# Kernel optimization log

Hardware: AMD Instinct MI355X
Metric: run time of the kernel (lower is better)

## Reference

```python
import jax, jax.numpy as jnp
import numpy as np

D_MODEL = 1024
NUM_HEADS = 16
HEAD_DIM = D_MODEL // NUM_HEADS
B, S, L_CACHE = 2, 1024, 1024


def setup_inputs() -> dict:
    key = jax.random.key(0)
    ks = jax.random.split(key, 12)
    sc = 1.0 / np.sqrt(D_MODEL)
    return {
        "x": jax.random.normal(ks[0], (B, S, D_MODEL), jnp.float32),
        "cache_k": jax.random.normal(ks[1], (B, NUM_HEADS, L_CACHE, HEAD_DIM), jnp.float32),
        "cache_v": jax.random.normal(ks[2], (B, NUM_HEADS, L_CACHE, HEAD_DIM), jnp.float32),
        "Wq": jax.random.normal(ks[3], (D_MODEL, D_MODEL), jnp.float32) * sc,
        "bq": jax.random.normal(ks[4], (D_MODEL,), jnp.float32) * 0.01,
        "Wk": jax.random.normal(ks[5], (D_MODEL, D_MODEL), jnp.float32) * sc,
        "bk": jax.random.normal(ks[6], (D_MODEL,), jnp.float32) * 0.01,
        "Wv": jax.random.normal(ks[7], (D_MODEL, D_MODEL), jnp.float32) * sc,
        "bv": jax.random.normal(ks[8], (D_MODEL,), jnp.float32) * 0.01,
        "Wo": jax.random.normal(ks[9], (D_MODEL, D_MODEL), jnp.float32) * sc,
        "bo": jax.random.normal(ks[10], (D_MODEL,), jnp.float32) * 0.01,
    }


def reference(x, cache_k, cache_v, Wq, bq, Wk, bk, Wv, bv, Wo, bo):
    b, s, d = x.shape
    h, hd = NUM_HEADS, HEAD_DIM
    # torch Linear: y = x @ W^T + b
    def proj(W, bias):
        y = jnp.einsum('bsd,ed->bse', x, W) + bias
        return y.reshape(b, s, h, hd).transpose(0, 2, 1, 3)  # [B,H,S,hd]
    Q = proj(Wq, bq)
    K = jnp.concatenate([cache_k, proj(Wk, bk)], axis=2)  # [B,H,T,hd]
    V = jnp.concatenate([cache_v, proj(Wv, bv)], axis=2)
    T = K.shape[2]
    scores = jnp.einsum('bhqd,bhkd->bhqk', Q, K) / jnp.sqrt(jnp.float32(hd))
    # causal mask with cache offset: query i sees keys j <= i + (T - s)
    offset = T - s
    q_idx = jnp.arange(s)[:, None]
    k_idx = jnp.arange(T)[None, :]
    mask = k_idx > (q_idx + offset)  # [S,T], True = masked
    scores = jnp.where(mask[None, None], -jnp.inf, scores)
    attn = jax.nn.softmax(scores, axis=-1)
    out = jnp.einsum('bhqk,bhkd->bhqd', attn, V)
    out = out.transpose(0, 2, 1, 3).reshape(b, s, d)
    return jnp.einsum('bsd,ed->bse', out, Wo) + bo
```

## Files before the change

### kernel.cpp

```cpp
#include <hip/hip_runtime.h>
#include <hip/hip_bf16.h>
#include <stdint.h>

typedef __bf16 bf16;
typedef __bf16 bf16x4 __attribute__((ext_vector_type(4)));
typedef __bf16 bf16x8 __attribute__((ext_vector_type(8)));
typedef float  f32x4  __attribute__((ext_vector_type(4)));

#define DEV __device__ __forceinline__

#define BB 2
#define HH 16
#define SS 1024
#define DD 1024
#define HD 64
#define LC 1024
#define TT 2048
#define OFFS 1024

DEV f32x4 mfma16(bf16x8 a, bf16x8 b, f32x4 c) {
    return __builtin_amdgcn_mfma_f32_16x16x32_bf16(a, b, c, 0, 0, 0);
}

DEV void async_load16(const bf16* g, bf16* lds) {
    auto gp = reinterpret_cast<const __attribute__((address_space(1))) void*>(
        reinterpret_cast<uintptr_t>(g));
    auto lp = reinterpret_cast<__attribute__((address_space(3))) void*>(
        reinterpret_cast<uintptr_t>(lds));
    __builtin_amdgcn_global_load_lds(gp, lp, 16, 0, 0);
}

__global__ __launch_bounds__(256) void cvt_all(
    const float* __restrict__ x,  bf16* __restrict__ xb,
    const float* __restrict__ w0, const float* __restrict__ w1,
    const float* __restrict__ w2, const float* __restrict__ w3,
    bf16* __restrict__ d0, bf16* __restrict__ d1,
    bf16* __restrict__ d2, bf16* __restrict__ d3,
    const float* __restrict__ ck, bf16* __restrict__ Kf,
    const float* __restrict__ cv, bf16* __restrict__ Vt) {
    __shared__ float tile[64][65];
    const int bid = blockIdx.x;
    const int tid = threadIdx.x;
    if (bid < 8192) {
        const float* s;
        bf16* d;
        int i;
        if (bid < 2048) {
            s = x; d = xb; i = bid * 256 + tid;
        } else if (bid < 6144) {
            int which = (bid - 2048) >> 10;
            s = which == 0 ? w0 : which == 1 ? w1 : which == 2 ? w2 : w3;
            d = which == 0 ? d0 : which == 1 ? d1 : which == 2 ? d2 : d3;
            i = ((bid - 2048) & 1023) * 256 + tid;
        } else {
            int ii = (bid - 6144) * 256 + tid;
            int bh  = ii >> 14;
            int rem = ii & 16383;
            float4 v = ((const float4*)ck)[ii];
            bf16x4 o;
            o[0] = (bf16)v.x; o[1] = (bf16)v.y; o[2] = (bf16)v.z; o[3] = (bf16)v.w;
            ((bf16x4*)(Kf + (size_t)bh * TT * HD))[rem] = o;
            return;
        }
        float4 v = ((const float4*)s)[i];
        bf16x4 o;
        o[0] = (bf16)v.x; o[1] = (bf16)v.y; o[2] = (bf16)v.z; o[3] = (bf16)v.w;
        ((bf16x4*)d)[i] = o;
    } else {
        int rem = bid - 8192;
        int bh = rem >> 4;
        int t0 = (rem & 15) * 64;
        int c4 = (tid & 15) * 4;
        int rr = tid >> 4;
        const float* src = cv + ((size_t)bh * LC + t0) * HD;
#pragma unroll
        for (int p = 0; p < 4; ++p) {
            int t = rr + p * 16;
            float4 v = *(const float4*)(src + (size_t)t * HD + c4);
            tile[c4 + 0][t] = v.x; tile[c4 + 1][t] = v.y;
            tile[c4 + 2][t] = v.z; tile[c4 + 3][t] = v.w;
        }
        __syncthreads();
        bf16* dst = Vt + (size_t)bh * HD * TT + t0;
#pragma unroll
        for (int p = 0; p < 4; ++p) {
            int d = rr + p * 16;
            int tc = (tid & 15) * 4;
            bf16x4 o;
            o[0] = (bf16)tile[d][tc + 0]; o[1] = (bf16)tile[d][tc + 1];
            o[2] = (bf16)tile[d][tc + 2]; o[3] = (bf16)tile[d][tc + 3];
            *(bf16x4*)(dst + (size_t)d * TT + tc) = o;
        }
    }
}

__global__ __launch_bounds__(256) void gemm_nt(
    const bf16* __restrict__ A, const bf16* __restrict__ W,
    const float* __restrict__ bq, const float* __restrict__ bk,
    const float* __restrict__ bv, const float* __restrict__ bo,
    bf16* __restrict__ Qb, bf16* __restrict__ Kf, bf16* __restrict__ Vt,
    float* __restrict__ Out, int is_oproj) {
    const int tid  = threadIdx.x;
    const int wv   = tid >> 6;
    const int lane = tid & 63;
    const int l16  = lane & 15;
    const int quad = lane >> 4;
    const int m0 = blockIdx.y * 64;
    const int n0 = blockIdx.x * 128;
    const int mode = is_oproj ? 3 : (n0 >> 10);
    const float* bias = (mode == 0) ? bq : (mode == 1) ? bk : (mode == 2) ? bv : bo;

    __shared__ __align__(16) bf16 As[2][64 * 64];
    __shared__ __align__(16) bf16 Bs[2][128 * 64];

    f32x4 acc[4][2];
#pragma unroll
    for (int i = 0; i < 4; ++i)
#pragma unroll
        for (int j = 0; j < 2; ++j) {
            f32x4 z = {0.f, 0.f, 0.f, 0.f};
            acc[i][j] = z;
        }

    auto stage = [&](int k0, int b) {
#pragma unroll
        for (int k = 0; k < 2; ++k) {
            int seg = k * 256 + tid;
            int row = seg >> 3;
            int c   = (seg & 7) ^ (row & 7);
            async_load16(A + (size_t)(m0 + row) * 1024 + k0 + c * 8, &As[b][seg * 8]);
        }
#pragma unroll
        for (int k = 0; k < 4; ++k) {
            int seg = k * 256 + tid;
            int row = seg >> 3;
            int c   = (seg & 7) ^ (row & 7);
            async_load16(W + (size_t)(n0 + row) * 1024 + k0 + c * 8, &Bs[b][seg * 8]);
        }
    };

    stage(0, 0);

    for (int it = 0; it < 16; ++it) {
        __syncthreads();
        const bf16* Ab = &As[it & 1][0];
        const bf16* Bb = &Bs[it & 1][0];
        if (it + 1 < 16) stage((it + 1) * 64, (it + 1) & 1);

#pragma unroll
        for (int kk = 0; kk < 2; ++kk) {
            bf16x8 af[4], bfr[2];
#pragma unroll
            for (int i = 0; i < 4; ++i) {
                int row = i * 16 + l16;
                int slot = (kk * 4 + quad) ^ (row & 7);
                af[i] = *(const bf16x8*)(Ab + (row * 8 + slot) * 8);
            }
#pragma unroll
            for (int j = 0; j < 2; ++j) {
                int row = wv * 32 + j * 16 + l16;
                int slot = (kk * 4 + quad) ^ (row & 7);
                bfr[j] = *(const bf16x8*)(Bb + (row * 8 + slot) * 8);
            }
#pragma unroll
            for (int i = 0; i < 4; ++i)
#pragma unroll
                for (int j = 0; j < 2; ++j)
                    acc[i][j] = mfma16(af[i], bfr[j], acc[i][j]);
        }
    }

#pragma unroll
    for (int i = 0; i < 4; ++i) {
#pragma unroll
        for (int j = 0; j < 2; ++j) {
            int n = n0 + wv * 32 + j * 16 + l16;
            float bval = bias[n & 1023];
#pragma unroll
            for (int r = 0; r < 4; ++r) {
                int m = m0 + i * 16 + quad * 4 + r;
                float v = acc[i][j][r] + bval;
                if (mode == 3) {
                    Out[(size_t)m * 1024 + n] = v;
                } else {
                    int b = m >> 10, s = m & 1023;
                    int h = (n & 1023) >> 6, d = n & 63;
                    int bh = b * HH + h;
                    if (mode == 0)
                        Qb[((size_t)bh * SS + s) * HD + d] = (bf16)v;
                    else if (mode == 1)
                        Kf[((size_t)bh * TT + LC + s) * HD + d] = (bf16)v;
                    else
                        Vt[((size_t)bh * HD + d) * TT + LC + s] = (bf16)v;
                }
            }
        }
    }
}

__global__ __launch_bounds__(256) void attn(const bf16* __restrict__ Qb,
                                            const bf16* __restrict__ Kf,
                                            const bf16* __restrict__ Vt,
                                            bf16* __restrict__ Ob) {
    const int i = blockIdx.x;
    const int bh = i & 31;
    const int qblk = (i < 256) ? (15 - (i >> 5)) : ((i >> 5) - 8);
    const int tid  = threadIdx.x;
    const int wv   = tid >> 6;
    const int qh   = wv & 1;
    const int kh   = wv >> 1;
    const int lane = tid & 63;
    const int l16  = lane & 15;
    const int quad = lane >> 4;
    const int qb   = qblk * 64;
    const int qw   = qb + qh * 32;
    const int kbase = kh * 64;

    const bf16* Qp = Qb + ((size_t)bh * SS + qw) * HD;
    const bf16* Kp = Kf + (size_t)bh * TT * HD;
    const bf16* Vp = Vt + (size_t)bh * HD * TT;

    __shared__ __align__(16) bf16 Ks[2][128 * 64];
    __shared__ __align__(16) bf16 Vs[2][64 * 128];

    bf16x8 qf[2][2];
#pragma unroll
    for (int qs = 0; qs < 2; ++qs)
#pragma unroll
        for (int dc = 0; dc < 2; ++dc)
            qf[qs][dc] = *(const bf16x8*)(Qp + (qs * 16 + l16) * HD + dc * 32 + quad * 8);

    float lsum[2] = {0.f, 0.f};
    f32x4 o[4][2];
#pragma unroll
    for (int dt = 0; dt < 4; ++dt)
#pragma unroll
        for (int qs = 0; qs < 2; ++qs) {
            f32x4 z = {0.f, 0.f, 0.f, 0.f};
            o[dt][qs] = z;
        }

    const int niters = qblk / 2 + 9;

    auto stage = [&](int tile, int b) {
        const int t0 = tile * 128;
#pragma unroll
        for (int j = 0; j < 4; ++j) {
            int seg = j * 256 + tid;
            int krow = seg >> 3;
            int kc   = (seg & 7) ^ (krow & 7);
            async_load16(Kp + (size_t)(t0 + krow) * HD + kc * 8, &Ks[b][seg * 8]);
            int drow = seg >> 4;
            int tc   = (seg & 15) ^ (drow & 15);
            async_load16(Vp + (size_t)drow * TT + t0 + tc * 8, &Vs[b][seg * 8]);
        }
    };

    stage(0, 0);

    const float C1 = 0.18033688f;
    const float C2 = -11.5415603f;

    for (int it = 0; it < niters; ++it) {
        __syncthreads();
        const bf16* Kb = &Ks[it & 1][0];
        const bf16* Vb = &Vs[it & 1][0];
        if (it + 1 < niters) stage(it + 1, (it + 1) & 1);

        const int t0 = it * 128;
        if (t0 + kbase > qw + 31 + OFFS) continue;
        const bool full = (t0 + kbase + 63 <= qw + OFFS);

        f32x4 s[4][2];
#pragma unroll
        for (int kt = 0; kt < 4; ++kt) {
            int row = kbase + kt * 16 + l16;
            int swz = row & 7;
            bf16x8 ka = *(const bf16x8*)(Kb + (row * 8 + (quad ^ swz)) * 8);
            bf16x8 kb = *(const bf16x8*)(Kb + (row * 8 + ((4 + quad) ^ swz)) * 8);
#pragma unroll
            for (int qs = 0; qs < 2; ++qs) {
                f32x4 z = {0.f, 0.f, 0.f, 0.f};
                z = mfma16(ka, qf[qs][0], z);
                z = mfma16(kb, qf[qs][1], z);
                s[kt][qs] = z;
            }
        }

        f32x4 p[4][2];
        if (full) {
#pragma unroll
            for (int kt = 0; kt < 4; ++kt)
#pragma unroll
                for (int qs = 0; qs < 2; ++qs)
#pragma unroll
                    for (int r = 0; r < 4; ++r)
                        p[kt][qs][r] = __builtin_amdgcn_exp2f(fmaf(s[kt][qs][r], C1, C2));
        } else {
#pragma unroll
            for (int qs = 0; qs < 2; ++qs) {
                const int qlim = qw + qs * 16 + l16 + OFFS - t0;
#pragma unroll
                for (int kt = 0; kt < 4; ++kt)
#pragma unroll
                    for (int r = 0; r < 4; ++r) {
                        int tl = kbase + kt * 16 + quad * 4 + r;
                        float e = __builtin_amdgcn_exp2f(fmaf(s[kt][qs][r], C1, C2));
                        p[kt][qs][r] = (tl <= qlim) ? e : 0.f;
                    }
            }
        }
#pragma unroll
        for (int qs = 0; qs < 2; ++qs)
#pragma unroll
            for (int kt = 0; kt < 4; ++kt)
                lsum[qs] += (p[kt][qs][0] + p[kt][qs][1]) + (p[kt][qs][2] + p[kt][qs][3]);

        bf16x8 pf[2][2];
#pragma unroll
        for (int kf = 0; kf < 2; ++kf)
#pragma unroll
            for (int qs = 0; qs < 2; ++qs)
#pragma unroll
                for (int j = 0; j < 4; ++j) {
                    pf[kf][qs][j]     = (bf16)p[kf * 2][qs][j];
                    pf[kf][qs][4 + j] = (bf16)p[kf * 2 + 1][qs][j];
                }

        const int q1 = quad >> 1;
        const int h4 = (quad & 1) * 4;
#pragma unroll
        for (int dt = 0; dt < 4; ++dt) {
            int row = dt * 16 + l16;
            int swz = row & 15;
#pragma unroll
            for (int kf = 0; kf < 2; ++kf) {
                int c0 = kh * 8 + kf * 4 + q1;
                bf16x4 v0 = *(const bf16x4*)(Vb + (row * 16 + (c0 ^ swz)) * 8 + h4);
                bf16x4 v1 = *(const bf16x4*)(Vb + (row * 16 + ((c0 + 2) ^ swz)) * 8 + h4);
                bf16x8 vf;
#pragma unroll
                for (int j = 0; j < 4; ++j) {
                    vf[j] = v0[j]; vf[4 + j] = v1[j];
                }
#pragma unroll
                for (int qs = 0; qs < 2; ++qs)
                    o[dt][qs] = mfma16(vf, pf[kf][qs], o[dt][qs]);
            }
        }
    }

#pragma unroll
    for (int qs = 0; qs < 2; ++qs) {
        lsum[qs] += __shfl_xor(lsum[qs], 16, 64);
        lsum[qs] += __shfl_xor(lsum[qs], 32, 64);
    }

    __syncthreads();
    float* So = (float*)&Ks[0][0];
    float* Sl = (float*)&Vs[0][0];
    if (kh == 1) {
#pragma unroll
        for (int dt = 0; dt < 4; ++dt)
#pragma unroll
            for (int qs = 0; qs < 2; ++qs)
#pragma unroll
                for (int r = 0; r < 4; ++r)
                    So[(dt * 8 + qs * 4 + r) * 128 + qh * 64 + lane] = o[dt][qs][r];
#pragma unroll
        for (int qs = 0; qs < 2; ++qs)
            Sl[qs * 128 + qh * 64 + lane] = lsum[qs];
    }
    __syncthreads();
    if (kh == 1) return;

#pragma unroll
    for (int dt = 0; dt < 4; ++dt)
#pragma unroll
        for (int qs = 0; qs < 2; ++qs)
#pragma unroll
            for (int r = 0; r < 4; ++r)
                o[dt][qs][r] += So[(dt * 8 + qs * 4 + r) * 128 + qh * 64 + lane];
    float rl[2];
#pragma unroll
    for (int qs = 0; qs < 2; ++qs)
        rl[qs] = 1.f / (lsum[qs] + Sl[qs * 128 + qh * 64 + lane]);

    const int b = bh >> 4, h = bh & 15;
#pragma unroll
    for (int qs = 0; qs < 2; ++qs) {
        const int q = qw + qs * 16 + l16;
        bf16* op = Ob + (((size_t)(b * SS + q) * HH) + h) * HD;
#pragma unroll
        for (int dt = 0; dt < 4; ++dt) {
            bf16x4 w;
#pragma unroll
            for (int r = 0; r < 4; ++r) w[r] = (bf16)(o[dt][qs][r] * rl[qs]);
            *(bf16x4*)(op + dt * 16 + quad * 4) = w;
        }
    }
}

extern "C" void kernel_launch(void* const* d_in, const int* in_sizes, int n_in,
                              void* d_out, int out_size, void* d_ws, size_t ws_size,
                              hipStream_t stream) {
    const float* x   = (const float*)d_in[0];
    const float* ck  = (const float*)d_in[1];
    const float* cv  = (const float*)d_in[2];
    const float* Wq  = (const float*)d_in[3];
    const float* bq  = (const float*)d_in[4];
    const float* Wk  = (const float*)d_in[5];
    const float* bk  = (const float*)d_in[6];
    const float* Wv  = (const float*)d_in[7];
    const float* bv  = (const float*)d_in[8];
    const float* Wo  = (const float*)d_in[9];
    const float* bo  = (const float*)d_in[10];
    float* out = (float*)d_out;

    char* ws = (char*)d_ws;
    bf16* xb  = (bf16*)(ws);
    bf16* wqb = (bf16*)(ws + ( 4u << 20));
    bf16* wkb = (bf16*)(ws + ( 6u << 20));
    bf16* wvb = (bf16*)(ws + ( 8u << 20));
    bf16* wob = (bf16*)(ws + (10u << 20));
    bf16* Qb  = (bf16*)(ws + (12u << 20));
    bf16* Kf  = (bf16*)(ws + (16u << 20));
    bf16* Vt  = (bf16*)(ws + (24u << 20));
    bf16* Ob  = (bf16*)(ws + (32u << 20));

    cvt_all<<<8704, 256, 0, stream>>>(x, xb, Wq, Wk, Wv, Wo, wqb, wkb, wvb, wob,
                                      ck, Kf, cv, Vt);

    gemm_nt<<<dim3(24, 32), 256, 0, stream>>>(xb, wqb, bq, bk, bv, bo,
                                              Qb, Kf, Vt, out, 0);
    attn<<<512, 256, 0, stream>>>(Qb, Kf, Vt, Ob);
    gemm_nt<<<dim3(8, 32), 256, 0, stream>>>(Ob, wob, bq, bk, bv, bo,
                                             Qb, Kf, Vt, out, 1);
}
```

Before: 159.5 us.

## Widen conversion vectors, add smaller-tile o-proj GEMM, simplify attention block order

The fp32-to-bf16 conversion kernel now handles eight elements per thread with 16-byte stores, which halves the number of blocks. The output projection moves to a dedicated kernel with 32-row tiles, so it launches twice as many blocks (512 instead of 256) to fill the GPU better. The projection-GEMM epilogue drops the o-proj branch. The attention block-to-query mapping changes from a zig-zag order to a plain descending order. That last change could alter load balance across the causal workload.

```diff
diff --git a/kernel.cpp b/kernel.cpp
--- a/kernel.cpp
+++ b/kernel.cpp
@@ -28,6 +28,13 @@
     auto lp = reinterpret_cast<__attribute__((address_space(3))) void*>(
         reinterpret_cast<uintptr_t>(lds));
     __builtin_amdgcn_global_load_lds(gp, lp, 16, 0, 0);
+}
+
+DEV bf16x8 cvt8(float4 a, float4 b) {
+    bf16x8 o;
+    o[0] = (bf16)a.x; o[1] = (bf16)a.y; o[2] = (bf16)a.z; o[3] = (bf16)a.w;
+    o[4] = (bf16)b.x; o[5] = (bf16)b.y; o[6] = (bf16)b.z; o[7] = (bf16)b.w;
+    return o;
 }
 
 __global__ __launch_bounds__(256) void cvt_all(
@@ -41,33 +48,31 @@
     __shared__ float tile[64][65];
     const int bid = blockIdx.x;
     const int tid = threadIdx.x;
-    if (bid < 8192) {
+    if (bid < 4096) {
         const float* s;
         bf16* d;
         int i;
-        if (bid < 2048) {
-            s = x; d = xb; i = bid * 256 + tid;
-        } else if (bid < 6144) {
-            int which = (bid - 2048) >> 10;
+        if (bid < 1024) {
+            s = x; d = xb; i = bid * 512 + tid * 2;
+        } else if (bid < 3072) {
+            int which = (bid - 1024) >> 9;
             s = which == 0 ? w0 : which == 1 ? w1 : which == 2 ? w2 : w3;
             d = which == 0 ? d0 : which == 1 ? d1 : which == 2 ? d2 : d3;
-            i = ((bid - 2048) & 1023) * 256 + tid;
+            i = ((bid - 1024) & 511) * 512 + tid * 2;
         } else {
-            int ii = (bid - 6144) * 256 + tid;
+            int ii = (bid - 3072) * 512 + tid * 2;
             int bh  = ii >> 14;
             int rem = ii & 16383;
-            float4 v = ((const float4*)ck)[ii];
-            bf16x4 o;
-            o[0] = (bf16)v.x; o[1] = (bf16)v.y; o[2] = (bf16)v.z; o[3] = (bf16)v.w;
-            ((bf16x4*)(Kf + (size_t)bh * TT * HD))[rem] = o;
+            float4 a = ((const float4*)ck)[ii];
+            float4 b = ((const float4*)ck)[ii + 1];
+            ((bf16x8*)(Kf + (size_t)bh * TT * HD))[rem >> 1] = cvt8(a, b);
             return;
         }
-        float4 v = ((const float4*)s)[i];
-        bf16x4 o;
-        o[0] = (bf16)v.x; o[1] = (bf16)v.y; o[2] = (bf16)v.z; o[3] = (bf16)v.w;
-        ((bf16x4*)d)[i] = o;
+        float4 a = ((const float4*)s)[i];
+        float4 b = ((const float4*)s)[i + 1];
+        ((bf16x8*)d)[i >> 1] = cvt8(a, b);
     } else {
-        int rem = bid - 8192;
+        int rem = bid - 4096;
         int bh = rem >> 4;
         int t0 = (rem & 15) * 64;
         int c4 = (tid & 15) * 4;
@@ -97,9 +102,8 @@
 __global__ __launch_bounds__(256) void gemm_nt(
     const bf16* __restrict__ A, const bf16* __restrict__ W,
     const float* __restrict__ bq, const float* __restrict__ bk,
-    const float* __restrict__ bv, const float* __restrict__ bo,
-    bf16* __restrict__ Qb, bf16* __restrict__ Kf, bf16* __restrict__ Vt,
-    float* __restrict__ Out, int is_oproj) {
+    const float* __restrict__ bv,
+    bf16* __restrict__ Qb, bf16* __restrict__ Kf, bf16* __restrict__ Vt) {
     const int tid  = threadIdx.x;
     const int wv   = tid >> 6;
     const int lane = tid & 63;
@@ -107,8 +111,8 @@
     const int quad = lane >> 4;
     const int m0 = blockIdx.y * 64;
     const int n0 = blockIdx.x * 128;
-    const int mode = is_oproj ? 3 : (n0 >> 10);
-    const float* bias = (mode == 0) ? bq : (mode == 1) ? bk : (mode == 2) ? bv : bo;
+    const int mode = n0 >> 10;
+    const float* bias = (mode == 0) ? bq : (mode == 1) ? bk : bv;
 
     __shared__ __align__(16) bf16 As[2][64 * 64];
     __shared__ __align__(16) bf16 Bs[2][128 * 64];
@@ -180,19 +184,100 @@
             for (int r = 0; r < 4; ++r) {
                 int m = m0 + i * 16 + quad * 4 + r;
                 float v = acc[i][j][r] + bval;
-                if (mode == 3) {
-                    Out[(size_t)m * 1024 + n] = v;
-                } else {
-                    int b = m >> 10, s = m & 1023;
-                    int h = (n & 1023) >> 6, d = n & 63;
-                    int bh = b * HH + h;
-                    if (mode == 0)
-                        Qb[((size_t)bh * SS + s) * HD + d] = (bf16)v;
-                    else if (mode == 1)
-                        Kf[((size_t)bh * TT + LC + s) * HD + d] = (bf16)v;
-                    else
-                        Vt[((size_t)bh * HD + d) * TT + LC + s] = (bf16)v;
-                }
+                int b = m >> 10, s = m & 1023;
+                int h = (n & 1023) >> 6, d = n & 63;
+                int bh = b * HH + h;
+                if (mode == 0)
+                    Qb[((size_t)bh * SS + s) * HD + d] = (bf16)v;
+                else if (mode == 1)
+                    Kf[((size_t)bh * TT + LC + s) * HD + d] = (bf16)v;
+                else
+                    Vt[((size_t)bh * HD + d) * TT + LC + s] = (bf16)v;
+            }
+        }
+    }
+}
+
+__global__ __launch_bounds__(256) void gemm_oproj(
+    const bf16* __restrict__ A, const bf16* __restrict__ W,
+    const float* __restrict__ bo, float* __restrict__ Out) {
+    const int tid  = threadIdx.x;
+    const int wv   = tid >> 6;
+    const int lane = tid & 63;
+    const int l16  = lane & 15;
+    const int quad = lane >> 4;
+    const int m0 = blockIdx.y * 32;
+    const int n0 = blockIdx.x * 128;
+
+    __shared__ __align__(16) bf16 As[2][32 * 64];
+    __shared__ __align__(16) bf16 Bs[2][128 * 64];
+
+    f32x4 acc[2][2];
+#pragma unroll
+    for (int i = 0; i < 2; ++i)
+#pragma unroll
+        for (int j = 0; j < 2; ++j) {
+            f32x4 z = {0.f, 0.f, 0.f, 0.f};
+            acc[i][j] = z;
+        }
+
+    auto stage = [&](int k0, int b) {
+        {
+            int seg = tid;
+            int row = seg >> 3;
+            int c   = (seg & 7) ^ (row & 7);
+            async_load16(A + (size_t)(m0 + row) * 1024 + k0 + c * 8, &As[b][seg * 8]);
+        }
+#pragma unroll
+        for (int k = 0; k < 4; ++k) {
+            int seg = k * 256 + tid;
+            int row = seg >> 3;
+            int c   = (seg & 7) ^ (row & 7);
+            async_load16(W + (size_t)(n0 + row) * 1024 + k0 + c * 8, &Bs[b][seg * 8]);
+        }
+    };
+
+    stage(0, 0);
+
+    for (int it = 0; it < 16; ++it) {
+        __syncthreads();
+        const bf16* Ab = &As[it & 1][0];
+        const bf16* Bb = &Bs[it & 1][0];
+        if (it + 1 < 16) stage((it + 1) * 64, (it + 1) & 1);
+
+#pragma unroll
+        for (int kk = 0; kk < 2; ++kk) {
+            bf16x8 af[2], bfr[2];
+#pragma unroll
+            for (int i = 0; i < 2; ++i) {
+                int row = i * 16 + l16;
+                int slot = (kk * 4 + quad) ^ (row & 7);
+                af[i] = *(const bf16x8*)(Ab + (row * 8 + slot) * 8);
+            }
+#pragma unroll
+            for (int j = 0; j < 2; ++j) {
+                int row = wv * 32 + j * 16 + l16;
+                int slot = (kk * 4 + quad) ^ (row & 7);
+                bfr[j] = *(const bf16x8*)(Bb + (row * 8 + slot) * 8);
+            }
+#pragma unroll
+            for (int i = 0; i < 2; ++i)
+#pragma unroll
+                for (int j = 0; j < 2; ++j)
+                    acc[i][j] = mfma16(af[i], bfr[j], acc[i][j]);
+        }
+    }
+
+#pragma unroll
+    for (int i = 0; i < 2; ++i) {
+#pragma unroll
+        for (int j = 0; j < 2; ++j) {
+            int n = n0 + wv * 32 + j * 16 + l16;
+            float bval = bo[n];
+#pragma unroll
+            for (int r = 0; r < 4; ++r) {
+                int m = m0 + i * 16 + quad * 4 + r;
+                Out[(size_t)m * 1024 + n] = acc[i][j][r] + bval;
             }
         }
     }
@@ -204,7 +289,7 @@
                                             bf16* __restrict__ Ob) {
     const int i = blockIdx.x;
     const int bh = i & 31;
-    const int qblk = (i < 256) ? (15 - (i >> 5)) : ((i >> 5) - 8);
+    const int qblk = 15 - (i >> 5);
     const int tid  = threadIdx.x;
     const int wv   = tid >> 6;
     const int qh   = wv & 1;
@@ -428,12 +513,10 @@
     bf16* Vt  = (bf16*)(ws + (24u << 20));
     bf16* Ob  = (bf16*)(ws + (32u << 20));
 
-    cvt_all<<<8704, 256, 0, stream>>>(x, xb, Wq, Wk, Wv, Wo, wqb, wkb, wvb, wob,
+    cvt_all<<<4608, 256, 0, stream>>>(x, xb, Wq, Wk, Wv, Wo, wqb, wkb, wvb, wob,
                                       ck, Kf, cv, Vt);
 
-    gemm_nt<<<dim3(24, 32), 256, 0, stream>>>(xb, wqb, bq, bk, bv, bo,
-                                              Qb, Kf, Vt, out, 0);
+    gemm_nt<<<dim3(24, 32), 256, 0, stream>>>(xb, wqb, bq, bk, bv, Qb, Kf, Vt);
     attn<<<512, 256, 0, stream>>>(Qb, Kf, Vt, Ob);
-    gemm_nt<<<dim3(8, 32), 256, 0, stream>>>(Ob, wob, bq, bk, bv, bo,
-                                             Qb, Kf, Vt, out, 1);
-}
+    gemm_oproj<<<dim3(8, 64), 256, 0, stream>>>(Ob, wob, bo, out);
+}
```

After: 157.9 us. About the same (-0.9%).
